# Performance work log

Hardware: AMD Instinct MI355X
Metric: run time of the kernel (lower is better)

The kernel has to match this reference:

```python
import jax, jax.numpy as jnp
import numpy as np

NUM_HEADS = 8
NUM_POINTS = 4
BS, BEV_RES, EMBED = 8, 128, 128


def setup_inputs() -> dict:
    key = jax.random.key(0)
    ks = jax.random.split(key, 8)
    Nq = BEV_RES * BEV_RES
    C = EMBED
    query = jax.random.normal(ks[0], (BS, Nq, C), jnp.float32)
    Wv = jax.random.normal(ks[1], (C, C), jnp.float32) * 0.05
    bv = jnp.zeros((C,), jnp.float32)
    Woff = jax.random.normal(ks[2], (C, NUM_HEADS * NUM_POINTS * 2), jnp.float32) * 0.02
    boff = jax.random.uniform(ks[3], (NUM_HEADS * NUM_POINTS * 2,), jnp.float32, -4.0, 4.0)
    Wattn = jax.random.normal(ks[4], (C, NUM_HEADS * NUM_POINTS), jnp.float32) * 0.02
    battn = jnp.zeros((NUM_HEADS * NUM_POINTS,), jnp.float32)
    Wout = jax.random.normal(ks[5], (C, C), jnp.float32) * 0.05
    bout = jnp.zeros((C,), jnp.float32)
    return {"query": query, "Wv": Wv, "bv": bv, "Woff": Woff, "boff": boff,
            "Wattn": Wattn, "battn": battn, "Wout": Wout, "bout": bout}


def reference(query, Wv, bv, Woff, boff, Wattn, battn, Wout, bout):
    bs, Nq, C = query.shape
    H, P = NUM_HEADS, NUM_POINTS
    hd = C // H
    R = int(np.sqrt(Nq))  # bev_res; value spatial map is R x R

    # BEV reference points: (x=col, y=row) normalized to [0,1], matching
    # np.meshgrid(linspace, linspace, indexing='ij') + stack((col,row),-1)
    lin = jnp.linspace(0.0, 1.0, R)
    col = jnp.tile(lin[None, :], (R, 1)).reshape(-1)
    row = jnp.tile(lin[:, None], (1, R)).reshape(-1)
    ref = jnp.stack([col, row], axis=-1)  # (Nq, 2)

    # projections (single level -> level axis squeezed)
    value = (query @ Wv + bv).reshape(bs, Nq, H, hd)
    off = (query @ Woff + boff).reshape(bs, Nq, H, P, 2)
    attn = jax.nn.softmax((query @ Wattn + battn).reshape(bs, Nq, H, P), axis=-1)

    # sampling locations, offsets normalized by [W, H] = [R, R]
    loc = ref[None, :, None, None, :] + off / R  # (bs, Nq, H, P, 2)

    # grid_sample semantics: bilinear, align_corners=False, zero padding
    x = loc[..., 0] * R - 0.5
    y = loc[..., 1] * R - 0.5
    x0f = jnp.floor(x)
    y0f = jnp.floor(y)
    wx1 = x - x0f
    wy1 = y - y0f
    x0 = x0f.astype(jnp.int32)
    y0 = y0f.astype(jnp.int32)
    x1 = x0 + 1
    y1 = y0 + 1

    vflat = value.transpose(0, 2, 1, 3)  # (bs, H, HW, hd), HW == Nq

    def tap(xi, yi, w):
        valid = (xi >= 0) & (xi < R) & (yi >= 0) & (yi < R)
        idx = jnp.clip(yi, 0, R - 1) * R + jnp.clip(xi, 0, R - 1)  # (bs, Nq, H, P)
        idx = idx.transpose(0, 2, 1, 3).reshape(bs, H, Nq * P)
        g = jnp.take_along_axis(vflat, idx[..., None], axis=2)  # (bs, H, Nq*P, hd)
        wm = (w * valid).transpose(0, 2, 1, 3).reshape(bs, H, Nq * P, 1)
        return g * wm

    sampled = (tap(x0, y0, (1.0 - wx1) * (1.0 - wy1))
               + tap(x1, y0, wx1 * (1.0 - wy1))
               + tap(x0, y1, (1.0 - wx1) * wy1)
               + tap(x1, y1, wx1 * wy1))  # (bs, H, Nq*P, hd)

    sampled = sampled.reshape(bs, H, Nq, P, hd)
    attn_t = attn.transpose(0, 2, 1, 3)  # (bs, H, Nq, P)
    out = (sampled * attn_t[..., None]).sum(axis=3)  # (bs, H, Nq, hd)
    out = out.transpose(0, 2, 1, 3).reshape(bs, Nq, C)
    out = out @ Wout + bout

    # mmcv MSDeformAttn adds identity (query) internally; SelfAttention adds residual again
    return out + query + query
```

## Files before the change

### kernel.cpp

```cpp
#include <hip/hip_runtime.h>
#include <hip/hip_bf16.h>

#define BS    8
#define NQ    16384
#define CDIM  128
#define NH    8
#define NPROJ 224
#define M_TOTAL (BS*NQ)

typedef __bf16 bf16_t;
typedef __bf16 bf16x8 __attribute__((ext_vector_type(8)));
typedef __bf16 bf16x4 __attribute__((ext_vector_type(4)));
typedef float  f32x4  __attribute__((ext_vector_type(4)));
typedef unsigned int u32;

__device__ __forceinline__ bf16x8 cvt_bf16x8(const float* p) {
    float4 a = *(const float4*)p;
    float4 b = *(const float4*)(p + 4);
    bf16x8 r;
    r[0] = (bf16_t)a.x; r[1] = (bf16_t)a.y; r[2] = (bf16_t)a.z; r[3] = (bf16_t)a.w;
    r[4] = (bf16_t)b.x; r[5] = (bf16_t)b.y; r[6] = (bf16_t)b.z; r[7] = (bf16_t)b.w;
    return r;
}
__device__ __forceinline__ float bflo(u32 d) { return __uint_as_float(d << 16); }
__device__ __forceinline__ float bfhi(u32 d) { return __uint_as_float(d & 0xffff0000u); }

__global__ void wtrans_kernel(const float* __restrict__ Wv, const float* __restrict__ Woff,
                              const float* __restrict__ Wattn, const float* __restrict__ Wout,
                              bf16_t* __restrict__ WT)
{
    const int i = blockIdx.x * 256 + threadIdx.x;
    const int n = i >> 7, k = i & 127;
    float v;
    if (n < 128)      v = Wv[k*128 + n];
    else if (n < 192) v = Woff[k*64 + (n-128)];
    else if (n < 224) v = Wattn[k*32 + (n-192)];
    else              v = Wout[k*128 + (n-224)];
    WT[i] = (bf16_t)v;
}

__global__ __launch_bounds__(512, 4)
void proj_kernel(const float* __restrict__ query, const bf16_t* __restrict__ WT,
                 const float* __restrict__ bv, const float* __restrict__ boff,
                 const float* __restrict__ battn,
                 bf16_t* __restrict__ value, bf16_t* __restrict__ offb,
                 bf16_t* __restrict__ attnb)
{
    __shared__ bf16_t Bt[NPROJ][136];
    __shared__ float  bias[NPROJ];
    const int t = threadIdx.x;

    for (int i = t; i < NPROJ*16; i += 512) {
        const int n = i >> 4, c = i & 15;
        *(bf16x8*)&Bt[n][c*8] = *(const bf16x8*)(WT + n*128 + c*8);
    }
    if (t < 128)      bias[t] = bv[t];
    else if (t < 192) bias[t] = boff[t-128];
    else if (t < 224) bias[t] = battn[t-192];
    __syncthreads();

    const int lane = t & 63;
    const int wave = t >> 6;
    const int ln   = lane & 15;
    const int q4   = lane >> 4;
    const int lk   = q4 * 8;

    const int row = blockIdx.x * 128 + wave * 16 + ln;
    const int b   = row >> 14;
    const int q   = row & (NQ - 1);

    bf16x8 qf[4];
    const float* ap = query + row * CDIM + lk;
    #pragma unroll
    for (int kc = 0; kc < 4; ++kc)
        qf[kc] = cvt_bf16x8(ap + kc*32);

    #pragma unroll 1
    for (int cb = 0; cb < 14; ++cb) {
        const int n0 = cb * 16;
        bf16x8 wf[4];
        const bf16_t* bp = &Bt[n0 + ln][lk];
        #pragma unroll
        for (int kc = 0; kc < 4; ++kc)
            wf[kc] = *(const bf16x8*)(bp + kc*32);

        f32x4 acc = {0.f, 0.f, 0.f, 0.f};
        #pragma unroll
        for (int kc = 0; kc < 4; ++kc)
            acc = __builtin_amdgcn_mfma_f32_16x16x32_bf16(wf[kc], qf[kc], acc, 0, 0, 0);

        const int c0 = n0 + q4*4;
        const f32x4 bi = *(const f32x4*)&bias[c0];
        bf16x4 s;
        #pragma unroll
        for (int r = 0; r < 4; ++r) s[r] = (bf16_t)(acc[r] + bi[r]);

        if (cb < 8) {
            const int h = c0 >> 4;
            *(bf16x4*)(value + (((size_t)(b*8 + h) << 14) + q)*16 + (c0 & 15)) = s;
        } else if (cb < 12) {
            *(bf16x4*)(offb + row*64 + (c0 - 128)) = s;
        } else {
            *(bf16x4*)(attnb + row*32 + (c0 - 192)) = s;
        }
    }
}

__global__ __launch_bounds__(512, 4)
void sample_out_kernel(const bf16_t* __restrict__ value, const bf16_t* __restrict__ offb,
                       const bf16_t* __restrict__ attnb, const bf16_t* __restrict__ WTo,
                       const float* __restrict__ bout, const float* __restrict__ query,
                       float* __restrict__ out)
{
    __shared__ bf16_t Wt[128][136];
    __shared__ float  bias[128];
    __shared__ bf16_t Srow[64][136];
    const int t = threadIdx.x;

    for (int i = t; i < 128*16; i += 512) {
        const int n = i >> 4, c = i & 15;
        *(bf16x8*)&Wt[n][c*8] = *(const bf16x8*)(WTo + n*128 + c*8);
    }
    if (t < 128) bias[t] = bout[t];

    const int row_base = blockIdx.x * 64;
    const int j   = t & 1;
    const int uq2 = t >> 1;

    #pragma unroll
    for (int u = 0; u < 2; ++u) {
        const int unit = u*256 + uq2;
        const int h    = unit >> 6;
        const int lr   = unit & 63;
        const int bq   = row_base + lr;
        const int q    = bq & (NQ - 1);
        const int b    = bq >> 14;

        union { bf16x4 v; u32 d[2]; } at;
        at.v = *(const bf16x4*)(attnb + bq*32 + h*4);
        float e0 = __expf(bflo(at.d[0])), e1 = __expf(bfhi(at.d[0]));
        float e2 = __expf(bflo(at.d[1])), e3 = __expf(bfhi(at.d[1]));
        float rs = 1.0f / (e0 + e1 + e2 + e3);
        const float aw[4] = {e0*rs, e1*rs, e2*rs, e3*rs};

        union { bf16x8 v; u32 d[4]; } of;
        of.v = *(const bf16x8*)(offb + bq*64 + h*8);

        const float bx = (float)(q & 127) * (128.0f/127.0f) - 0.5f;
        const float by = (float)(q >> 7)  * (128.0f/127.0f) - 0.5f;

        const bf16_t* vbase = value + ((size_t)(b*8 + h) << 14)*16 + j*8;

        float a[8] = {0.f,0.f,0.f,0.f,0.f,0.f,0.f,0.f};
        #pragma unroll
        for (int p = 0; p < 4; ++p) {
            float x = bx + bflo(of.d[p]);
            float y = by + bfhi(of.d[p]);
            float xf = floorf(x), yf = floorf(y);
            int   x0 = (int)xf,  y0 = (int)yf;
            float wx1 = x - xf, wy1 = y - yf;
            float wxe0 = (((unsigned)x0       < 128u) ? (1.0f - wx1) : 0.f);
            float wxe1 = (((unsigned)(x0 + 1) < 128u) ? wx1          : 0.f);
            float wye0 = (((unsigned)y0       < 128u) ? (1.0f - wy1) : 0.f) * aw[p];
            float wye1 = (((unsigned)(y0 + 1) < 128u) ? wy1          : 0.f) * aw[p];
            int xc0 = min(max(x0, 0), 127),      xc1 = min(max(x0 + 1, 0), 127);
            int rb0 = min(max(y0, 0), 127) << 7, rb1 = min(max(y0 + 1, 0), 127) << 7;

            const int   idx[4] = {rb0 + xc0, rb0 + xc1, rb1 + xc0, rb1 + xc1};
            const float wt [4] = {wxe0*wye0, wxe1*wye0, wxe0*wye1, wxe1*wye1};
            #pragma unroll
            for (int tp = 0; tp < 4; ++tp) {
                const uint4 d = *(const uint4*)(vbase + ((size_t)idx[tp] << 4));
                const float w = wt[tp];
                a[0] += w * bflo(d.x); a[1] += w * bfhi(d.x);
                a[2] += w * bflo(d.y); a[3] += w * bfhi(d.y);
                a[4] += w * bflo(d.z); a[5] += w * bfhi(d.z);
                a[6] += w * bflo(d.w); a[7] += w * bfhi(d.w);
            }
        }
        bf16x8 s;
        #pragma unroll
        for (int r = 0; r < 8; ++r) s[r] = (bf16_t)a[r];
        *(bf16x8*)(&Srow[lr][h*16 + j*8]) = s;
    }
    __syncthreads();

    const int lane = t & 63;
    const int wave = t >> 6;
    const int ln   = lane & 15;
    const int q4   = lane >> 4;
    const int lk   = q4 * 8;
    const int rt   = wave >> 1;
    const int cb0  = (wave & 1) * 4;

    bf16x8 sf[4];
    const bf16_t* sp = &Srow[rt*16 + ln][lk];
    #pragma unroll
    for (int kc = 0; kc < 4; ++kc)
        sf[kc] = *(const bf16x8*)(sp + kc*32);

    const int grow = row_base + rt*16 + ln;

    #pragma unroll
    for (int c = 0; c < 4; ++c) {
        const int n0 = (cb0 + c) * 16;
        bf16x8 wf[4];
        const bf16_t* bp = &Wt[n0 + ln][lk];
        #pragma unroll
        for (int kc = 0; kc < 4; ++kc)
            wf[kc] = *(const bf16x8*)(bp + kc*32);

        f32x4 acc = {0.f, 0.f, 0.f, 0.f};
        #pragma unroll
        for (int kc = 0; kc < 4; ++kc)
            acc = __builtin_amdgcn_mfma_f32_16x16x32_bf16(wf[kc], sf[kc], acc, 0, 0, 0);

        const int c0 = n0 + q4*4;
        const f32x4 bi = *(const f32x4*)&bias[c0];
        const float4 qv = *(const float4*)(query + grow*CDIM + c0);
        float4 o;
        o.x = acc[0] + bi[0] + 2.0f*qv.x;
        o.y = acc[1] + bi[1] + 2.0f*qv.y;
        o.z = acc[2] + bi[2] + 2.0f*qv.z;
        o.w = acc[3] + bi[3] + 2.0f*qv.w;
        *(float4*)(out + grow*CDIM + c0) = o;
    }
}

extern "C" void kernel_launch(void* const* d_in, const int* in_sizes, int n_in,
                              void* d_out, int out_size, void* d_ws, size_t ws_size,
                              hipStream_t stream)
{
    const float* query = (const float*)d_in[0];
    const float* Wv    = (const float*)d_in[1];
    const float* bv    = (const float*)d_in[2];
    const float* Woff  = (const float*)d_in[3];
    const float* boff  = (const float*)d_in[4];
    const float* Wattn = (const float*)d_in[5];
    const float* battn = (const float*)d_in[6];
    const float* Wout  = (const float*)d_in[7];
    const float* bout  = (const float*)d_in[8];
    float* out = (float*)d_out;

    bf16_t* value = (bf16_t*)d_ws;
    bf16_t* offb  = (bf16_t*)((char*)d_ws + (size_t)M_TOTAL*CDIM*2);
    bf16_t* attnb = (bf16_t*)((char*)d_ws + (size_t)M_TOTAL*CDIM*2 + (size_t)M_TOTAL*64*2);
    bf16_t* WT    = (bf16_t*)((char*)d_ws + (size_t)M_TOTAL*CDIM*2 + (size_t)M_TOTAL*64*2
                                          + (size_t)M_TOTAL*32*2);
    bf16_t* WTo   = WT + 224*128;

    wtrans_kernel<<<(352*128)/256, 256, 0, stream>>>(Wv, Woff, Wattn, Wout, WT);
    proj_kernel<<<M_TOTAL/128, 512, 0, stream>>>(query, WT, bv, boff, battn,
                                                 value, offb, attnb);
    sample_out_kernel<<<M_TOTAL/64, 512, 0, stream>>>(value, offb, attnb,
                                                      WTo, bout, query, out);
}
```

Measured before the change: 192.6 us.

## Process two row groups per proj block, head-major offset/attn layout, one thread per head

```diff
diff --git a/kernel.cpp b/kernel.cpp
--- a/kernel.cpp
+++ b/kernel.cpp
@@ -65,15 +65,16 @@
     const int q4   = lane >> 4;
     const int lk   = q4 * 8;
 
-    const int row = blockIdx.x * 128 + wave * 16 + ln;
-    const int b   = row >> 14;
-    const int q   = row & (NQ - 1);
-
-    bf16x8 qf[4];
-    const float* ap = query + row * CDIM + lk;
+    const int row0 = blockIdx.x * 256 + wave * 16 + ln;
+
+    bf16x8 qf[2][4];
     #pragma unroll
-    for (int kc = 0; kc < 4; ++kc)
-        qf[kc] = cvt_bf16x8(ap + kc*32);
+    for (int g = 0; g < 2; ++g) {
+        const float* ap = query + (row0 + g*128) * CDIM + lk;
+        #pragma unroll
+        for (int kc = 0; kc < 4; ++kc)
+            qf[g][kc] = cvt_bf16x8(ap + kc*32);
+    }
 
     #pragma unroll 1
     for (int cb = 0; cb < 14; ++cb) {
@@ -84,29 +85,43 @@
         for (int kc = 0; kc < 4; ++kc)
             wf[kc] = *(const bf16x8*)(bp + kc*32);
 
-        f32x4 acc = {0.f, 0.f, 0.f, 0.f};
-        #pragma unroll
-        for (int kc = 0; kc < 4; ++kc)
-            acc = __builtin_amdgcn_mfma_f32_16x16x32_bf16(wf[kc], qf[kc], acc, 0, 0, 0);
+        f32x4 acc0 = {0.f, 0.f, 0.f, 0.f};
+        f32x4 acc1 = {0.f, 0.f, 0.f, 0.f};
+        #pragma unroll
+        for (int kc = 0; kc < 4; ++kc) {
+            acc0 = __builtin_amdgcn_mfma_f32_16x16x32_bf16(wf[kc], qf[0][kc], acc0, 0, 0, 0);
+            acc1 = __builtin_amdgcn_mfma_f32_16x16x32_bf16(wf[kc], qf[1][kc], acc1, 0, 0, 0);
+        }
 
         const int c0 = n0 + q4*4;
         const f32x4 bi = *(const f32x4*)&bias[c0];
-        bf16x4 s;
-        #pragma unroll
-        for (int r = 0; r < 4; ++r) s[r] = (bf16_t)(acc[r] + bi[r]);
-
-        if (cb < 8) {
-            const int h = c0 >> 4;
-            *(bf16x4*)(value + (((size_t)(b*8 + h) << 14) + q)*16 + (c0 & 15)) = s;
-        } else if (cb < 12) {
-            *(bf16x4*)(offb + row*64 + (c0 - 128)) = s;
-        } else {
-            *(bf16x4*)(attnb + row*32 + (c0 - 192)) = s;
+
+        #pragma unroll
+        for (int g = 0; g < 2; ++g) {
+            const f32x4 acc = g ? acc1 : acc0;
+            const int row = row0 + g*128;
+            const int b   = row >> 14;
+            const int q   = row & (NQ - 1);
+            bf16x4 s;
+            #pragma unroll
+            for (int r = 0; r < 4; ++r) s[r] = (bf16_t)(acc[r] + bi[r]);
+
+            if (cb < 8) {
+                const int h = c0 >> 4;
+                *(bf16x4*)(value + (((size_t)(b*8 + h) << 14) + q)*16 + (c0 & 15)) = s;
+            } else if (cb < 12) {
+                const int h    = (c0 - 128) >> 3;
+                const int part = (c0 - 128) & 7;
+                *(bf16x4*)(offb + (((size_t)(b*8 + h) << 14) + q)*8 + part) = s;
+            } else {
+                const int h = (c0 - 192) >> 2;
+                *(bf16x4*)(attnb + (((size_t)(b*8 + h) << 14) + q)*4) = s;
+            }
         }
     }
 }
 
-__global__ __launch_bounds__(512, 4)
+__global__ __launch_bounds__(512, 6)
 void sample_out_kernel(const bf16_t* __restrict__ value, const bf16_t* __restrict__ offb,
                        const bf16_t* __restrict__ attnb, const bf16_t* __restrict__ WTo,
                        const float* __restrict__ bout, const float* __restrict__ query,
@@ -124,34 +139,33 @@
     if (t < 128) bias[t] = bout[t];
 
     const int row_base = blockIdx.x * 64;
-    const int j   = t & 1;
-    const int uq2 = t >> 1;
-
-    #pragma unroll
-    for (int u = 0; u < 2; ++u) {
-        const int unit = u*256 + uq2;
-        const int h    = unit >> 6;
-        const int lr   = unit & 63;
-        const int bq   = row_base + lr;
-        const int q    = bq & (NQ - 1);
-        const int b    = bq >> 14;
+    {
+        const int h  = t >> 6;
+        const int lr = t & 63;
+        const int bq = row_base + lr;
+        const int q  = bq & (NQ - 1);
+        const int b  = bq >> 14;
+        const size_t plane = (size_t)(b*8 + h) << 14;
 
         union { bf16x4 v; u32 d[2]; } at;
-        at.v = *(const bf16x4*)(attnb + bq*32 + h*4);
+        at.v = *(const bf16x4*)(attnb + (plane + q)*4);
         float e0 = __expf(bflo(at.d[0])), e1 = __expf(bfhi(at.d[0]));
         float e2 = __expf(bflo(at.d[1])), e3 = __expf(bfhi(at.d[1]));
         float rs = 1.0f / (e0 + e1 + e2 + e3);
         const float aw[4] = {e0*rs, e1*rs, e2*rs, e3*rs};
 
         union { bf16x8 v; u32 d[4]; } of;
-        of.v = *(const bf16x8*)(offb + bq*64 + h*8);
+        of.v = *(const bf16x8*)(offb + (plane + q)*8);
 
         const float bx = (float)(q & 127) * (128.0f/127.0f) - 0.5f;
         const float by = (float)(q >> 7)  * (128.0f/127.0f) - 0.5f;
 
-        const bf16_t* vbase = value + ((size_t)(b*8 + h) << 14)*16 + j*8;
-
-        float a[8] = {0.f,0.f,0.f,0.f,0.f,0.f,0.f,0.f};
+        const bf16_t* vbase = value + plane*16;
+
+        float a[16];
+        #pragma unroll
+        for (int r = 0; r < 16; ++r) a[r] = 0.f;
+
         #pragma unroll
         for (int p = 0; p < 4; ++p) {
             float x = bx + bflo(of.d[p]);
@@ -170,18 +184,25 @@
             const float wt [4] = {wxe0*wye0, wxe1*wye0, wxe0*wye1, wxe1*wye1};
             #pragma unroll
             for (int tp = 0; tp < 4; ++tp) {
-                const uint4 d = *(const uint4*)(vbase + ((size_t)idx[tp] << 4));
+                const bf16_t* pp = vbase + ((size_t)idx[tp] << 4);
+                const uint4 dA = *(const uint4*)pp;
+                const uint4 dB = *(const uint4*)(pp + 8);
                 const float w = wt[tp];
-                a[0] += w * bflo(d.x); a[1] += w * bfhi(d.x);
-                a[2] += w * bflo(d.y); a[3] += w * bfhi(d.y);
-                a[4] += w * bflo(d.z); a[5] += w * bfhi(d.z);
-                a[6] += w * bflo(d.w); a[7] += w * bfhi(d.w);
+                a[0]  += w * bflo(dA.x); a[1]  += w * bfhi(dA.x);
+                a[2]  += w * bflo(dA.y); a[3]  += w * bfhi(dA.y);
+                a[4]  += w * bflo(dA.z); a[5]  += w * bfhi(dA.z);
+                a[6]  += w * bflo(dA.w); a[7]  += w * bfhi(dA.w);
+                a[8]  += w * bflo(dB.x); a[9]  += w * bfhi(dB.x);
+                a[10] += w * bflo(dB.y); a[11] += w * bfhi(dB.y);
+                a[12] += w * bflo(dB.z); a[13] += w * bfhi(dB.z);
+                a[14] += w * bflo(dB.w); a[15] += w * bfhi(dB.w);
             }
         }
-        bf16x8 s;
-        #pragma unroll
-        for (int r = 0; r < 8; ++r) s[r] = (bf16_t)a[r];
-        *(bf16x8*)(&Srow[lr][h*16 + j*8]) = s;
+        bf16x8 s0, s1;
+        #pragma unroll
+        for (int r = 0; r < 8; ++r) { s0[r] = (bf16_t)a[r]; s1[r] = (bf16_t)a[8+r]; }
+        *(bf16x8*)(&Srow[lr][h*16])     = s0;
+        *(bf16x8*)(&Srow[lr][h*16 + 8]) = s1;
     }
     __syncthreads();
 
@@ -250,7 +271,7 @@
     bf16_t* WTo   = WT + 224*128;
 
     wtrans_kernel<<<(352*128)/256, 256, 0, stream>>>(Wv, Woff, Wattn, Wout, WT);
-    proj_kernel<<<M_TOTAL/128, 512, 0, stream>>>(query, WT, bv, boff, battn,
+    proj_kernel<<<M_TOTAL/256, 512, 0, stream>>>(query, WT, bv, boff, battn,
                                                  value, offb, attnb);
     sample_out_kernel<<<M_TOTAL/64, 512, 0, stream>>>(value, offb, attnb,
                                                       WTo, bout, query, out);
```

Result: slower. 474.2 us (+146.1%).

## Double rows per projection block, head-major offset/attn layout, swizzle sample blocks

Applied to the files above, without the earlier changes.

```diff
diff --git a/kernel.cpp b/kernel.cpp
--- a/kernel.cpp
+++ b/kernel.cpp
@@ -65,15 +65,16 @@
     const int q4   = lane >> 4;
     const int lk   = q4 * 8;
 
-    const int row = blockIdx.x * 128 + wave * 16 + ln;
-    const int b   = row >> 14;
-    const int q   = row & (NQ - 1);
-
-    bf16x8 qf[4];
-    const float* ap = query + row * CDIM + lk;
-    #pragma unroll
-    for (int kc = 0; kc < 4; ++kc)
-        qf[kc] = cvt_bf16x8(ap + kc*32);
+    const int row0 = blockIdx.x * 256 + wave * 16 + ln;
+
+    bf16x8 qf[2][4];
+    #pragma unroll
+    for (int g = 0; g < 2; ++g) {
+        const float* ap = query + (row0 + g*128) * CDIM + lk;
+        #pragma unroll
+        for (int kc = 0; kc < 4; ++kc)
+            qf[g][kc] = cvt_bf16x8(ap + kc*32);
+    }
 
     #pragma unroll 1
     for (int cb = 0; cb < 14; ++cb) {
@@ -84,24 +85,38 @@
         for (int kc = 0; kc < 4; ++kc)
             wf[kc] = *(const bf16x8*)(bp + kc*32);
 
-        f32x4 acc = {0.f, 0.f, 0.f, 0.f};
-        #pragma unroll
-        for (int kc = 0; kc < 4; ++kc)
-            acc = __builtin_amdgcn_mfma_f32_16x16x32_bf16(wf[kc], qf[kc], acc, 0, 0, 0);
+        f32x4 acc0 = {0.f, 0.f, 0.f, 0.f};
+        f32x4 acc1 = {0.f, 0.f, 0.f, 0.f};
+        #pragma unroll
+        for (int kc = 0; kc < 4; ++kc) {
+            acc0 = __builtin_amdgcn_mfma_f32_16x16x32_bf16(wf[kc], qf[0][kc], acc0, 0, 0, 0);
+            acc1 = __builtin_amdgcn_mfma_f32_16x16x32_bf16(wf[kc], qf[1][kc], acc1, 0, 0, 0);
+        }
 
         const int c0 = n0 + q4*4;
         const f32x4 bi = *(const f32x4*)&bias[c0];
-        bf16x4 s;
-        #pragma unroll
-        for (int r = 0; r < 4; ++r) s[r] = (bf16_t)(acc[r] + bi[r]);
-
-        if (cb < 8) {
-            const int h = c0 >> 4;
-            *(bf16x4*)(value + (((size_t)(b*8 + h) << 14) + q)*16 + (c0 & 15)) = s;
-        } else if (cb < 12) {
-            *(bf16x4*)(offb + row*64 + (c0 - 128)) = s;
-        } else {
-            *(bf16x4*)(attnb + row*32 + (c0 - 192)) = s;
+
+        #pragma unroll
+        for (int g = 0; g < 2; ++g) {
+            const f32x4 acc = g ? acc1 : acc0;
+            const int row = row0 + g*128;
+            const int b   = row >> 14;
+            const int q   = row & (NQ - 1);
+            bf16x4 s;
+            #pragma unroll
+            for (int r = 0; r < 4; ++r) s[r] = (bf16_t)(acc[r] + bi[r]);
+
+            if (cb < 8) {
+                const int h = c0 >> 4;
+                *(bf16x4*)(value + (((size_t)(b*8 + h) << 14) + q)*16 + (c0 & 15)) = s;
+            } else if (cb < 12) {
+                const int h    = (c0 - 128) >> 3;
+                const int part = (c0 - 128) & 7;
+                *(bf16x4*)(offb + (((size_t)(b*8 + h) << 14) + q)*8 + part) = s;
+            } else {
+                const int h = (c0 - 192) >> 2;
+                *(bf16x4*)(attnb + (((size_t)(b*8 + h) << 14) + q)*4) = s;
+            }
         }
     }
 }
@@ -123,7 +138,9 @@
     }
     if (t < 128) bias[t] = bout[t];
 
-    const int row_base = blockIdx.x * 64;
+    const int swz      = ((blockIdx.x & 7) << 8) + (blockIdx.x >> 3);
+    const int row_base = swz * 64;
+
     const int j   = t & 1;
     const int uq2 = t >> 1;
 
@@ -135,21 +152,22 @@
         const int bq   = row_base + lr;
         const int q    = bq & (NQ - 1);
         const int b    = bq >> 14;
+        const size_t plane = (size_t)(b*8 + h) << 14;
 
         union { bf16x4 v; u32 d[2]; } at;
-        at.v = *(const bf16x4*)(attnb + bq*32 + h*4);
+        at.v = *(const bf16x4*)(attnb + (plane + q)*4);
         float e0 = __expf(bflo(at.d[0])), e1 = __expf(bfhi(at.d[0]));
         float e2 = __expf(bflo(at.d[1])), e3 = __expf(bfhi(at.d[1]));
         float rs = 1.0f / (e0 + e1 + e2 + e3);
         const float aw[4] = {e0*rs, e1*rs, e2*rs, e3*rs};
 
         union { bf16x8 v; u32 d[4]; } of;
-        of.v = *(const bf16x8*)(offb + bq*64 + h*8);
+        of.v = *(const bf16x8*)(offb + (plane + q)*8);
 
         const float bx = (float)(q & 127) * (128.0f/127.0f) - 0.5f;
         const float by = (float)(q >> 7)  * (128.0f/127.0f) - 0.5f;
 
-        const bf16_t* vbase = value + ((size_t)(b*8 + h) << 14)*16 + j*8;
+        const bf16_t* vbase = value + plane*16 + j*8;
 
         float a[8] = {0.f,0.f,0.f,0.f,0.f,0.f,0.f,0.f};
         #pragma unroll
@@ -250,7 +268,7 @@
     bf16_t* WTo   = WT + 224*128;
 
     wtrans_kernel<<<(352*128)/256, 256, 0, stream>>>(Wv, Woff, Wattn, Wout, WT);
-    proj_kernel<<<M_TOTAL/128, 512, 0, stream>>>(query, WT, bv, boff, battn,
+    proj_kernel<<<M_TOTAL/256, 512, 0, stream>>>(query, WT, bv, boff, battn,
                                                  value, offb, attnb);
     sample_out_kernel<<<M_TOTAL/64, 512, 0, stream>>>(value, offb, attnb,
                                                       WTo, bout, query, out);
```

Result: faster. 183.2 us (-4.9%).
